# Performance work log

Measured on AMD Instinct MI355X. Metric: run time of the kernel, lower is better.

The kernel has to match this reference:

```python
import jax, jax.numpy as jnp
import numpy as np

B, L, D = 16, 512, 512
T, P = 4096, 4


def setup_inputs() -> dict:
    key = jax.random.key(0)
    k1, k2, k3, k4 = jax.random.split(key, 4)
    encoder_outputs = jax.random.normal(k1, (B, L, D), dtype=jnp.float32)
    durations = jax.random.randint(k2, (B, L), 0, 8, dtype=jnp.int32)
    frames_positions = jax.random.normal(k3, (B, T, P), dtype=jnp.float32)
    input_lengths = jax.random.randint(k4, (B,), 0, L, dtype=jnp.int32)
    return {
        "encoder_outputs": encoder_outputs,
        "durations": durations,
        "frames_positions": frames_positions,
        "input_lengths": input_lengths,
    }


def reference(encoder_outputs, durations, frames_positions, input_lengths):
    # encoder_outputs: [B, L, D], durations: [B, L] int, frames_positions: [B, T, P]
    Bn, Ln, Dn = encoder_outputs.shape
    Tn = frames_positions.shape[1]
    cum = jnp.cumsum(durations, axis=1)  # [B, L] inclusive cumsum of durations
    t = jnp.arange(Tn)

    def expand_one(enc, c):
        # frame t maps to token j with cum[j-1] <= t < cum[j]
        idx = jnp.searchsorted(c, t, side="right")          # [T]
        valid = t < c[-1]                                     # frames beyond total stay zero
        gathered = enc[jnp.clip(idx, 0, Ln - 1)]              # [T, D]
        return jnp.where(valid[:, None], gathered, jnp.zeros((), enc.dtype))

    expanded = jax.vmap(expand_one)(encoder_outputs, cum)     # [B, T, D]
    return jnp.concatenate([expanded, frames_positions], axis=2)  # [B, T, D+P]
```

## Files before the change

kernel.cpp:

```cpp
#include <hip/hip_runtime.h>

constexpr int Bn = 16;
constexpr int Ln = 512;
constexpr int Dn = 512;
constexpr int Tn = 4096;
constexpr int Pn = 4;

constexpr int D4     = Dn / 4;
constexpr int ROW_F4 = (Dn + Pn) / 4;
constexpr int NROWS  = Bn * Tn;
constexpr int NXCD   = 8;

__global__ __launch_bounds__(Ln) void cum_kernel(
    const int* __restrict__ durations, int* __restrict__ cum_out) {
    const int b = blockIdx.x;
    const int l = threadIdx.x;

    __shared__ int cum[Ln];
    cum[l] = durations[b * Ln + l];
    __syncthreads();
    for (int off = 1; off < Ln; off <<= 1) {
        int v = (l >= off) ? cum[l - off] : 0;
        __syncthreads();
        cum[l] += v;
        __syncthreads();
    }
    cum_out[b * Ln + l] = cum[l];
}

constexpr int THREADS   = 256;
constexpr int F4T       = 4;
constexpr int F4B       = THREADS * F4T;
constexpr int NBLK_FILL = NROWS * D4 / F4B;
constexpr int BPX_FILL  = NBLK_FILL / NXCD;

__global__ __launch_bounds__(THREADS) void fill_kernel(
    const float4* __restrict__ fpos4, const int* __restrict__ cum,
    float4* __restrict__ out4) {
    const int xcd  = blockIdx.x & (NXCD - 1);
    const int j    = blockIdx.x >> 3;
    const int blk  = xcd * BPX_FILL + j;
    const int base = blk * F4B + threadIdx.x;
    const int b    = blk >> 9;
    const int total = cum[b * Ln + (Ln - 1)];

    #pragma unroll
    for (int h = 0; h < F4T; ++h) {
        const int g   = base + h * THREADS;
        const int row = g >> 7;
        const int t   = row & (Tn - 1);
        if (t >= total)
            out4[g + row] = make_float4(0.f, 0.f, 0.f, 0.f);
    }

    if (threadIdx.x < 8) {
        const int r = blk * 8 + threadIdx.x;
        out4[r * ROW_F4 + (ROW_F4 - 1)] = fpos4[r];
    }
}

constexpr int NBLK_COPY = Bn * Ln / 2;
constexpr int BPX_COPY  = NBLK_COPY / NXCD;

__global__ __launch_bounds__(THREADS) void copy_kernel(
    const float4* __restrict__ enc4, const int* __restrict__ cum,
    float4* __restrict__ out4) {
    const int xcd  = blockIdx.x & (NXCD - 1);
    const int j    = blockIdx.x >> 3;
    const int blk  = xcd * BPX_COPY + j;
    const int b    = blk >> 8;
    const int wave = threadIdx.x >> 6;
    const int lane = threadIdx.x & 63;
    const int tok  = ((blk & 255) << 1) + (wave >> 1);
    const int col  = ((wave & 1) << 6) + lane;

    int start = (tok == 0) ? 0 : cum[b * Ln + tok - 1];
    int end   = cum[b * Ln + tok];
    if (end > Tn) end = Tn;
    if (start >= end) return;

    const float4 v = enc4[(((b << 9) + tok) << 7) + col];

    const int rbase = b * Tn;
    for (int d = start; d < end; ++d)
        out4[(rbase + d) * ROW_F4 + col] = v;
}

extern "C" void kernel_launch(void* const* d_in, const int* in_sizes, int n_in,
                              void* d_out, int out_size, void* d_ws, size_t ws_size,
                              hipStream_t stream) {
    const float* enc  = (const float*)d_in[0];
    const int*   dur  = (const int*)d_in[1];
    const float* fpos = (const float*)d_in[2];

    float* out = (float*)d_out;
    int* cum = (int*)d_ws;

    cum_kernel<<<Bn, Ln, 0, stream>>>(dur, cum);

    static_assert(NBLK_FILL % NXCD == 0 && NBLK_COPY % NXCD == 0, "sizing");
    static_assert(F4B == 8 * D4, "fill block must cover exactly 8 rows");

    fill_kernel<<<NBLK_FILL, THREADS, 0, stream>>>(
        (const float4*)fpos, cum, (float4*)out);
    copy_kernel<<<NBLK_COPY, THREADS, 0, stream>>>(
        (const float4*)enc, cum, (float4*)out);
}
```

Baseline: 161.1 us.

## Fuse scan, fill and copy into one kernel with per-block prefix reduction

Replaces the separate cumsum, zero-fill and copy kernels with a single launch. Each copy block recomputes the prefix sum of durations before its token via a block-wide shuffle reduction, and each fill block recomputes the total duration, so the workspace cumsum array and inter-kernel dependencies disappear. This removes two launch boundaries and lets fill and copy work overlap in one grid, at the cost of redundant reads of the durations row per block.

```diff
diff --git a/kernel.cpp b/kernel.cpp
--- a/kernel.cpp
+++ b/kernel.cpp
@@ -10,80 +10,88 @@
 constexpr int ROW_F4 = (Dn + Pn) / 4;
 constexpr int NROWS  = Bn * Tn;
 constexpr int NXCD   = 8;
+constexpr int THREADS = 256;
 
-__global__ __launch_bounds__(Ln) void cum_kernel(
-    const int* __restrict__ durations, int* __restrict__ cum_out) {
-    const int b = blockIdx.x;
-    const int l = threadIdx.x;
+constexpr int NBLK_COPY = Bn * Ln / 2;
+constexpr int BPX_COPY  = NBLK_COPY / NXCD;
 
-    __shared__ int cum[Ln];
-    cum[l] = durations[b * Ln + l];
-    __syncthreads();
-    for (int off = 1; off < Ln; off <<= 1) {
-        int v = (l >= off) ? cum[l - off] : 0;
-        __syncthreads();
-        cum[l] += v;
-        __syncthreads();
-    }
-    cum_out[b * Ln + l] = cum[l];
-}
-
-constexpr int THREADS   = 256;
 constexpr int F4T       = 4;
 constexpr int F4B       = THREADS * F4T;
 constexpr int NBLK_FILL = NROWS * D4 / F4B;
 constexpr int BPX_FILL  = NBLK_FILL / NXCD;
 
-__global__ __launch_bounds__(THREADS) void fill_kernel(
-    const float4* __restrict__ fpos4, const int* __restrict__ cum,
-    float4* __restrict__ out4) {
-    const int xcd  = blockIdx.x & (NXCD - 1);
-    const int j    = blockIdx.x >> 3;
-    const int blk  = xcd * BPX_FILL + j;
-    const int base = blk * F4B + threadIdx.x;
-    const int b    = blk >> 9;
-    const int total = cum[b * Ln + (Ln - 1)];
+constexpr int NBLK = NBLK_COPY + NBLK_FILL;
 
-    #pragma unroll
-    for (int h = 0; h < F4T; ++h) {
-        const int g   = base + h * THREADS;
-        const int row = g >> 7;
-        const int t   = row & (Tn - 1);
-        if (t >= total)
-            out4[g + row] = make_float4(0.f, 0.f, 0.f, 0.f);
+__global__ __launch_bounds__(THREADS) void fused_kernel(
+    const float4* __restrict__ enc4, const float4* __restrict__ fpos4,
+    const int* __restrict__ dur, float4* __restrict__ out4) {
+    __shared__ int s_red[4];
+    const int tid  = threadIdx.x;
+    const int wave = tid >> 6;
+    const int lane = tid & 63;
+    const int gid  = blockIdx.x;
+
+    if (gid < NBLK_COPY) {
+        const int xcd  = gid & (NXCD - 1);
+        const int j    = gid >> 3;
+        const int blk  = xcd * BPX_COPY + j;
+        const int b    = blk >> 8;
+        const int tok0 = (blk & 255) << 1;
+        const int* db  = dur + b * Ln;
+
+        int acc = 0;
+        if (tid < tok0)       acc += db[tid];
+        if (tid + 256 < tok0) acc += db[tid + 256];
+        #pragma unroll
+        for (int off = 32; off; off >>= 1) acc += __shfl_xor(acc, off);
+        if (lane == 0) s_red[wave] = acc;
+        __syncthreads();
+        const int S  = s_red[0] + s_red[1] + s_red[2] + s_red[3];
+        const int d0 = db[tok0];
+        const int d1 = db[tok0 + 1];
+
+        const int tp  = wave >> 1;
+        const int tok = tok0 + tp;
+        const int col = ((wave & 1) << 6) | lane;
+        int start = S + (tp ? d0 : 0);
+        int end   = start + (tp ? d1 : d0);
+        if (end > Tn) end = Tn;
+        if (start < end) {
+            const float4 v = enc4[(((b << 9) + tok) << 7) + col];
+            const int rbase = b * Tn;
+            for (int d = start; d < end; ++d)
+                out4[(rbase + d) * ROW_F4 + col] = v;
+        }
+    } else {
+        const int g2  = gid - NBLK_COPY;
+        const int xcd = g2 & (NXCD - 1);
+        const int j   = g2 >> 3;
+        const int blk = xcd * BPX_FILL + j;
+        const int b   = blk >> 9;
+        const int* db = dur + b * Ln;
+
+        int acc = db[tid] + db[tid + 256];
+        #pragma unroll
+        for (int off = 32; off; off >>= 1) acc += __shfl_xor(acc, off);
+        if (lane == 0) s_red[wave] = acc;
+        __syncthreads();
+        const int total = s_red[0] + s_red[1] + s_red[2] + s_red[3];
+
+        const int base = blk * F4B + tid;
+        #pragma unroll
+        for (int h = 0; h < F4T; ++h) {
+            const int g   = base + h * THREADS;
+            const int row = g >> 7;
+            const int t   = row & (Tn - 1);
+            if (t >= total)
+                out4[g + row] = make_float4(0.f, 0.f, 0.f, 0.f);
+        }
+
+        if (tid < 8) {
+            const int r = blk * 8 + tid;
+            out4[r * ROW_F4 + (ROW_F4 - 1)] = fpos4[r];
+        }
     }
-
-    if (threadIdx.x < 8) {
-        const int r = blk * 8 + threadIdx.x;
-        out4[r * ROW_F4 + (ROW_F4 - 1)] = fpos4[r];
-    }
-}
-
-constexpr int NBLK_COPY = Bn * Ln / 2;
-constexpr int BPX_COPY  = NBLK_COPY / NXCD;
-
-__global__ __launch_bounds__(THREADS) void copy_kernel(
-    const float4* __restrict__ enc4, const int* __restrict__ cum,
-    float4* __restrict__ out4) {
-    const int xcd  = blockIdx.x & (NXCD - 1);
-    const int j    = blockIdx.x >> 3;
-    const int blk  = xcd * BPX_COPY + j;
-    const int b    = blk >> 8;
-    const int wave = threadIdx.x >> 6;
-    const int lane = threadIdx.x & 63;
-    const int tok  = ((blk & 255) << 1) + (wave >> 1);
-    const int col  = ((wave & 1) << 6) + lane;
-
-    int start = (tok == 0) ? 0 : cum[b * Ln + tok - 1];
-    int end   = cum[b * Ln + tok];
-    if (end > Tn) end = Tn;
-    if (start >= end) return;
-
-    const float4 v = enc4[(((b << 9) + tok) << 7) + col];
-
-    const int rbase = b * Tn;
-    for (int d = start; d < end; ++d)
-        out4[(rbase + d) * ROW_F4 + col] = v;
 }
 
 extern "C" void kernel_launch(void* const* d_in, const int* in_sizes, int n_in,
@@ -92,17 +100,11 @@
     const float* enc  = (const float*)d_in[0];
     const int*   dur  = (const int*)d_in[1];
     const float* fpos = (const float*)d_in[2];
+    float* out = (float*)d_out;
 
-    float* out = (float*)d_out;
-    int* cum = (int*)d_ws;
-
-    cum_kernel<<<Bn, Ln, 0, stream>>>(dur, cum);
-
-    static_assert(NBLK_FILL % NXCD == 0 && NBLK_COPY % NXCD == 0, "sizing");
+    static_assert(NBLK_COPY % NXCD == 0 && NBLK_FILL % NXCD == 0, "sizing");
     static_assert(F4B == 8 * D4, "fill block must cover exactly 8 rows");
 
-    fill_kernel<<<NBLK_FILL, THREADS, 0, stream>>>(
-        (const float4*)fpos, cum, (float4*)out);
-    copy_kernel<<<NBLK_COPY, THREADS, 0, stream>>>(
-        (const float4*)enc, cum, (float4*)out);
+    fused_kernel<<<NBLK, THREADS, 0, stream>>>(
+        (const float4*)enc, (const float4*)fpos, dur, (float4*)out);
 }
```

Measured after the change: 154.8 us. -3.9%, faster.
